# Kernel optimization log

Hardware: AMD Instinct MI355X
Metric: run time of the kernel (lower is better)

The kernel has to match this reference:

```python
import jax, jax.numpy as jnp
import numpy as np

K = 20          # hardcoded in get_graph_feature
EPS = 1e-5      # BatchNorm2d default eps


def bn(x, g, b):
    # training-mode batch norm over all axes except channel (last axis), biased var
    ax = tuple(range(x.ndim - 1))
    m = x.mean(axis=ax, keepdims=True)
    v = x.var(axis=ax, keepdims=True)
    return (x - m) * jax.lax.rsqrt(v + EPS) * g + b


def knn_idx(x):
    # x: (B, C, N) -> (B, N, K) indices of K nearest neighbors (incl. self)
    xt = jnp.swapaxes(x, 1, 2)                      # (B, N, C)
    inner = -2.0 * jnp.einsum('bnc,bmc->bnm', xt, xt)
    xx = jnp.sum(x * x, axis=1)                     # (B, N)
    neg_dist = -xx[:, :, None] - inner - xx[:, None, :]   # (B, N, N)
    _, idx = jax.lax.top_k(neg_dist, K)
    return idx


def graph_feature(x):
    # x: (B, C, N) -> (B, N, K, 2C)  [neighbor feats, center feats]
    idx = knn_idx(x)
    xt = jnp.swapaxes(x, 1, 2)                      # (B, N, C)
    B = x.shape[0]
    nb = xt[jnp.arange(B)[:, None, None], idx]      # (B, N, K, C)
    ctr = jnp.broadcast_to(xt[:, :, None, :], nb.shape)
    return jnp.concatenate([nb, ctr], axis=-1)


def setup_inputs() -> dict:
    key = jax.random.key(0)
    ks = jax.random.split(key, 12)
    B, C, N = 8, 3, 4096
    EMB = 512

    def w(k, cin, cout):
        return jax.random.normal(k, (cin, cout), dtype=jnp.float32) * np.float32(1.0 / np.sqrt(cin))

    return {
        'x': jax.random.normal(ks[0], (B, C, N), dtype=jnp.float32),
        'W1': w(ks[1], 2 * C, 64),
        'W2': w(ks[2], 64, 64),
        'W3': w(ks[3], 64, 128),
        'W4': w(ks[4], 128, 256),
        'W5': w(ks[5], 512, EMB),
        'g1': jnp.ones((64,), jnp.float32),  'b1': jnp.zeros((64,), jnp.float32),
        'g2': jnp.ones((64,), jnp.float32),  'b2': jnp.zeros((64,), jnp.float32),
        'g3': jnp.ones((128,), jnp.float32), 'b3': jnp.zeros((128,), jnp.float32),
        'g4': jnp.ones((256,), jnp.float32), 'b4': jnp.zeros((256,), jnp.float32),
        'g5': jnp.ones((EMB,), jnp.float32), 'b5': jnp.zeros((EMB,), jnp.float32),
    }


def reference(x, W1, W2, W3, W4, W5, g1, b1, g2, b2, g3, b3, g4, b4, g5, b5):
    f = graph_feature(x)                              # (B, N, K, 6)
    h = jax.nn.relu(bn(f @ W1, g1, b1))               # (B, N, K, 64)
    x1 = h.max(axis=2)                                # (B, N, 64)
    h = jax.nn.relu(bn(h @ W2, g2, b2))
    x2 = h.max(axis=2)
    h = jax.nn.relu(bn(h @ W3, g3, b3))
    x3 = h.max(axis=2)
    h = jax.nn.relu(bn(h @ W4, g4, b4))
    x4 = h.max(axis=2)                                # (B, N, 256)
    cat = jnp.concatenate([x1, x2, x3, x4], axis=-1)  # (B, N, 512)
    out = jax.nn.relu(bn(cat @ W5, g5, b5))           # (B, N, 512); last_relu=True
    return jnp.swapaxes(out, 1, 2)                    # (B, 512, N)
```

## Files before the change

### kernel.cpp

```cpp
#include <hip/hip_runtime.h>
#include <hip/hip_bf16.h>
#include <cfloat>

using bf16 = __hip_bfloat16;

typedef short short8 __attribute__((ext_vector_type(8)));
typedef float floatx16 __attribute__((ext_vector_type(16)));
union Frag { short8 v; uint2 u2[2]; };
union FragQ { short8 v; uint4 q; uint2 u2[2]; };
union U4b { uint4 q; unsigned short s[8]; };

constexpr int Bb = 8, Nn = 4096, Kk = 20;
constexpr int BN = Bb * Nn;
constexpr int Mrows = BN * Kk;
constexpr float EPSf = 1e-5f;

static __device__ __forceinline__ float b2f(bf16 v){ return __bfloat162float(v); }
static __device__ __forceinline__ bf16 f2b(float v){ return __float2bfloat16(v); }
static __device__ __forceinline__ unsigned short f2bu(float v){
  union { bf16 b; unsigned short u; } cv; cv.b = __float2bfloat16(v); return cv.u;
}
static __device__ __forceinline__ float bits2f(unsigned short u){
  union { unsigned int i; float f; } c; c.i = ((unsigned)u)<<16; return c.f;
}

__global__ void zero_kernel(float* __restrict__ p, int n){
  int i = blockIdx.x*256 + threadIdx.x;
  if (i < n) p[i] = 0.f;
}

__global__ void w3t_kernel(const float* __restrict__ W3f, bf16* __restrict__ W3T){
  int id = blockIdx.x*256 + threadIdx.x;
  if (id >= 128*64) return;
  int n = id >> 6, k = id & 63;
  W3T[id] = f2b(W3f[(size_t)k*128 + n]);
}

__global__ void w4t_kernel(const float* __restrict__ W4f, bf16* __restrict__ W4T){
  int id = blockIdx.x*256 + threadIdx.x;
  if (id >= 128*256) return;
  int k = id >> 8, c = id & 255;
  W4T[(size_t)c*128 + k] = f2b(W4f[id]);
}

__global__ void w5t_kernel(const float* __restrict__ W5f, bf16* __restrict__ W5T){
  int id = blockIdx.x*256 + threadIdx.x;
  if (id >= 512*512) return;
  int k = id >> 9, c = id & 511;
  W5T[(size_t)c*512 + k] = f2b(W5f[id]);
}

__global__ __launch_bounds__(256) void knnA_kernel(const float* __restrict__ x,
                                                   float* __restrict__ pv, int* __restrict__ pi){
#pragma clang fp contract(off)
  __shared__ float4 p4[512];
  __shared__ unsigned short lst[256*62];
  int blk = blockIdx.x;
  int stripe = blk & 7;
  int chunk  = (blk >> 3) & 15;
  int b      = blk >> 7;
  const float* xb = x + b*3*Nn;
  int j0 = stripe*512;
  for (int u = threadIdx.x; u < 512; u += 256){
    int j = j0 + u;
    float a0 = xb[j];
    float a1 = xb[Nn + j];
    float a2 = xb[2*Nn + j];
    float s = a0*a0; s = s + a1*a1; s = s + a2*a2;
    p4[u] = make_float4(a0, a1, a2, s);
  }
  __syncthreads();
  int i = chunk*256 + threadIdx.x;
  float xi = xb[i], yi = xb[Nn+i], zi = xb[2*Nn+i];
  float ni = xi*xi; ni = ni + yi*yi; ni = ni + zi*zi;
  float mni = -ni;
  float xi2 = xi + xi, yi2 = yi + yi, zi2 = zi + zi;
  float bv[13];
  #pragma unroll
  for (int s=0;s<13;++s) bv[s] = FLT_MAX;
  for (int g=0; g<32; ++g){
    float gm = -FLT_MAX;
    #pragma unroll
    for (int e=0;e<16;++e){
      float4 p = p4[g*16+e];
      float base = mni - p.w;
      float nd = fmaf(xi2, p.x, fmaf(yi2, p.y, fmaf(zi2, p.z, base)));
      gm = fmaxf(gm, nd);
    }
    #pragma unroll
    for (int s=12; s>=1; --s)
      bv[s] = fminf(bv[s], fmaxf(bv[s-1], gm));
    bv[0] = fminf(bv[0], gm);
  }
  float thr = bv[12];
  thr = thr - (fabsf(thr)*1e-5f + 1e-6f);
  unsigned short* ml = &lst[threadIdx.x*62];
  int cnt = 0;
  for (int u=0; u<512; ++u){
    float4 p = p4[u];
    float base = mni - p.w;
    float nd = fmaf(xi2, p.x, fmaf(yi2, p.y, fmaf(zi2, p.z, base)));
    if (nd >= thr && cnt < 60){ ml[cnt] = (unsigned short)u; ++cnt; }
  }
  float av[Kk]; int ai[Kk];
  #pragma unroll
  for (int s=0;s<Kk;++s){ av[s] = -FLT_MAX; ai[s] = 0; }
  if (cnt >= 60){
    for (int u=0; u<512; ++u){
      float4 p = p4[u];
      float dot = xi*p.x; dot = dot + yi*p.y; dot = dot + zi*p.z;
      float inner = -2.0f*dot;
      float nd = mni - inner; nd = nd - p.w;
      if (nd > av[Kk-1]){
        #pragma unroll
        for (int s=Kk-1; s>=1; --s){
          bool cs = nd > av[s];
          bool cp = nd > av[s-1];
          av[s] = cs ? (cp ? av[s-1] : nd) : av[s];
          ai[s] = cs ? (cp ? ai[s-1] : (j0+u)) : ai[s];
        }
        if (nd > av[0]){ av[0] = nd; ai[0] = j0+u; }
      }
    }
  } else {
    for (int t=0; t<cnt; ++t){
      int lj = ml[t];
      float4 p = p4[lj];
      float dot = xi*p.x; dot = dot + yi*p.y; dot = dot + zi*p.z;
      float inner = -2.0f*dot;
      float nd = mni - inner; nd = nd - p.w;
      if (nd > av[Kk-1]){
        #pragma unroll
        for (int s=Kk-1; s>=1; --s){
          bool cs = nd > av[s];
          bool cp = nd > av[s-1];
          av[s] = cs ? (cp ? av[s-1] : nd) : av[s];
          ai[s] = cs ? (cp ? ai[s-1] : (j0+lj)) : ai[s];
        }
        if (nd > av[0]){ av[0] = nd; ai[0] = j0+lj; }
      }
    }
  }
  long long base = ((long long)(b*Nn + i)*8 + stripe)*Kk;
  #pragma unroll
  for (int s=0;s<Kk;++s){ pv[base+s] = av[s]; pi[base+s] = ai[s]; }
}

__global__ __launch_bounds__(256) void knnB_kernel(const float* __restrict__ pv,
                                                   const int* __restrict__ pi,
                                                   const float* __restrict__ x,
                                                   int* __restrict__ idx,
                                                   float* __restrict__ part){
  int p = blockIdx.x*256 + threadIdx.x;
  long long base = (long long)p*8*Kk;
  float av[Kk]; int ai[Kk];
  #pragma unroll
  for (int s=0;s<Kk;++s){ av[s]=pv[base+s]; ai[s]=pi[base+s]; }
  for (int t=Kk; t<8*Kk; ++t){
    float nd = pv[base+t]; int j = pi[base+t];
    if (nd > av[Kk-1]){
      #pragma unroll
      for (int s=Kk-1;s>=1;--s){
        bool cs = nd > av[s];
        bool cp = nd > av[s-1];
        av[s] = cs ? (cp?av[s-1]:nd) : av[s];
        ai[s] = cs ? (cp?ai[s-1]:j) : ai[s];
      }
      if (nd > av[0]){ av[0]=nd; ai[0]=j; }
    }
  }
  #pragma unroll
  for (int s=0;s<Kk;++s) idx[(long long)p*Kk+s] = ai[s];
  int b = p >> 12, n = p & 4095;
  const float* xb = x + b*3*Nn;
  float cx = xb[n], cy = xb[Nn+n], cz = xb[2*Nn+n];
  float snx=0.f, sny=0.f, snz=0.f;
  float a00=0.f,a01=0.f,a02=0.f,a11=0.f,a12=0.f,a22=0.f;
  #pragma unroll
  for (int s=0;s<Kk;++s){
    int j = ai[s];
    float nx = xb[j], ny = xb[Nn+j], nz = xb[2*Nn+j];
    snx += nx; sny += ny; snz += nz;
    a00 = fmaf(nx,nx,a00); a01 = fmaf(nx,ny,a01); a02 = fmaf(nx,nz,a02);
    a11 = fmaf(ny,ny,a11); a12 = fmaf(ny,nz,a12); a22 = fmaf(nz,nz,a22);
  }
  float acc[36];
  acc[0]=a00;  acc[1]=a01;  acc[2]=a02;
  acc[6]=a01;  acc[7]=a11;  acc[8]=a12;
  acc[12]=a02; acc[13]=a12; acc[14]=a22;
  acc[3]=snx*cx;  acc[4]=snx*cy;  acc[5]=snx*cz;
  acc[9]=sny*cx;  acc[10]=sny*cy; acc[11]=sny*cz;
  acc[15]=snz*cx; acc[16]=snz*cy; acc[17]=snz*cz;
  acc[18]=cx*snx; acc[19]=cx*sny; acc[20]=cx*snz;
  acc[24]=cy*snx; acc[25]=cy*sny; acc[26]=cy*snz;
  acc[30]=cz*snx; acc[31]=cz*sny; acc[32]=cz*snz;
  float k20 = (float)Kk;
  acc[21]=k20*cx*cx; acc[22]=k20*cx*cy; acc[23]=k20*cx*cz;
  acc[27]=k20*cy*cx; acc[28]=k20*cy*cy; acc[29]=k20*cy*cz;
  acc[33]=k20*cz*cx; acc[34]=k20*cz*cy; acc[35]=k20*cz*cz;
  float s6[6] = { snx, sny, snz, k20*cx, k20*cy, k20*cz };
  __shared__ float red[256];
  #pragma unroll
  for (int v=0; v<42; ++v){
    red[threadIdx.x] = (v<36)? acc[v] : s6[v-36];
    __syncthreads();
    for (int s=128; s>0; s>>=1){
      if (threadIdx.x < s) red[threadIdx.x] += red[threadIdx.x+s];
      __syncthreads();
    }
    if (threadIdx.x==0) part[blockIdx.x*48 + v] = red[0];
    __syncthreads();
  }
}

__global__ void reducef_kernel(const float* __restrict__ part, float* __restrict__ Gf,
                               float* __restrict__ sumf){
  int t = threadIdx.x;
  if (t < 42){
    float s = 0.f;
    for (int i=0;i<128;++i) s += part[i*48 + t];
    if (t<36) Gf[t]=s; else sumf[t-36]=s;
  }
}

__global__ __launch_bounds__(256) void gram3_kernel(const bf16* __restrict__ H, int M,
                                                    float* __restrict__ G,
                                                    float* __restrict__ sumh){
  __shared__ short HTa[64*68];
  __shared__ float csum[64];
  int tid = threadIdx.x, lane = tid & 63, w = tid >> 6;
  if (tid < 64) csum[tid] = 0.f;
  int nchunks = gridDim.x;
  int rpc = M / nchunks;
  int r0 = blockIdx.x*rpc;
  int mt = w >> 1, nt = w & 1;
  floatx16 acc;
  #pragma unroll
  for (int q=0;q<16;++q) acc[q]=0.f;
  int arow = (mt*32 + (lane&31))*68;
  int brow = (nt*32 + (lane&31))*68;
  int ko = (lane>>5)*8;
  int c0s = (tid & 7)*8;
  float cs[8];
  #pragma unroll
  for (int j=0;j<8;++j) cs[j]=0.f;
  for (int rb=r0; rb<r0+rpc; rb+=64){
    #pragma unroll
    for (int s=0;s<2;++s){
      int e = tid + s*256;
      int row = e >> 3;
      U4b va; va.q = *(const uint4*)&H[(size_t)(rb+row)*64 + c0s];
      #pragma unroll
      for (int j=0;j<8;++j){
        HTa[(c0s+j)*68 + row] = (short)va.s[j];
        cs[j] += bits2f(va.s[j]);
      }
    }
    __syncthreads();
    #pragma unroll
    for (int kc=0;kc<64;kc+=16){
      Frag a, b;
      const short* ap = &HTa[arow + kc + ko];
      const short* bp = &HTa[brow + kc + ko];
      a.u2[0] = *(const uint2*)ap;  a.u2[1] = *(const uint2*)(ap+4);
      b.u2[0] = *(const uint2*)bp;  b.u2[1] = *(const uint2*)(bp+4);
      acc = __builtin_amdgcn_mfma_f32_32x32x16_bf16(a.v, b.v, acc, 0, 0, 0);
    }
    __syncthreads();
  }
  int col = lane & 31, rbase = 4*(lane>>5);
  #pragma unroll
  for (int r=0;r<16;++r){
    int row = (r&3) + 8*(r>>2) + rbase;
    atomicAdd(&G[(size_t)(mt*32 + row)*64 + nt*32 + col], acc[r]);
  }
  #pragma unroll
  for (int j=0;j<8;++j) atomicAdd(&csum[c0s+j], cs[j]);
  __syncthreads();
  if (tid < 64) atomicAdd(&sumh[tid], csum[tid]);
}

__global__ __launch_bounds__(256) void gram5_kernel(const bf16* __restrict__ H,
                                                    float* __restrict__ G,
                                                    float* __restrict__ sumh){
  __shared__ short HTa[128*68];
  __shared__ short HTb[128*68];
  __shared__ float csum[128];
  int blk = blockIdx.x;
  int pair = blk & 15;
  int chunk = blk >> 4;
  int tr = pair >> 2, tc = pair & 3;
  bool diag = (tr == tc);
  int tid = threadIdx.x, lane = tid & 63, w = tid >> 6;
  if (tid < 128) csum[tid] = 0.f;
  int rpc = BN / 32;
  int r0 = chunk*rpc;
  int pl = lane & 31, ko = (lane>>5)*8, rbase = 4*(lane>>5);
  int mt = w;
  int arow = (mt*32 + pl)*68;
  floatx16 acc[4];
  #pragma unroll
  for (int nt=0;nt<4;++nt)
    #pragma unroll
    for (int q=0;q<16;++q) acc[nt][q]=0.f;
  int c0s = (tid & 15)*8;
  float cs[8];
  #pragma unroll
  for (int j=0;j<8;++j) cs[j]=0.f;
  const short* Bbase = diag ? HTa : HTb;
  for (int rb=r0; rb<r0+rpc; rb+=64){
    #pragma unroll
    for (int s=0;s<4;++s){
      int e = tid + s*256;
      int row = e >> 4;
      U4b va; va.q = *(const uint4*)&H[(size_t)(rb+row)*512 + tr*128 + c0s];
      #pragma unroll
      for (int j=0;j<8;++j) HTa[(c0s+j)*68 + row] = (short)va.s[j];
      if (diag){
        #pragma unroll
        for (int j=0;j<8;++j) cs[j] += bits2f(va.s[j]);
      } else {
        U4b vb; vb.q = *(const uint4*)&H[(size_t)(rb+row)*512 + tc*128 + c0s];
        #pragma unroll
        for (int j=0;j<8;++j) HTb[(c0s+j)*68 + row] = (short)vb.s[j];
      }
    }
    __syncthreads();
    #pragma unroll
    for (int kc=0;kc<64;kc+=16){
      Frag a;
      const short* ap = &HTa[arow + kc + ko];
      a.u2[0] = *(const uint2*)ap;  a.u2[1] = *(const uint2*)(ap+4);
      #pragma unroll
      for (int nt=0;nt<4;++nt){
        Frag b;
        const short* bp = &Bbase[(nt*32 + pl)*68 + kc + ko];
        b.u2[0] = *(const uint2*)bp;  b.u2[1] = *(const uint2*)(bp+4);
        acc[nt] = __builtin_amdgcn_mfma_f32_32x32x16_bf16(a.v, b.v, acc[nt], 0, 0, 0);
      }
    }
    __syncthreads();
  }
  #pragma unroll
  for (int nt=0;nt<4;++nt){
    #pragma unroll
    for (int r=0;r<16;++r){
      int row = (r&3) + 8*(r>>2) + rbase;
      atomicAdd(&G[(size_t)(tr*128 + mt*32 + row)*512 + tc*128 + nt*32 + pl], acc[nt][r]);
    }
  }
  if (diag){
    #pragma unroll
    for (int j=0;j<8;++j) atomicAdd(&csum[c0s+j], cs[j]);
    __syncthreads();
    if (tid < 128) atomicAdd(&sumh[tr*128 + tid], csum[tid]);
  }
}

__global__ void kP_kernel(const float* __restrict__ G, const float* __restrict__ Wf,
                          float* __restrict__ P, int Cin, int Cout){
  int id = blockIdx.x*256 + threadIdx.x;
  if (id >= Cin*Cout) return;
  int i = id / Cout, j = id - i*Cout;
  float s = 0.f;
  for (int k=0;k<Cin;++k) s = fmaf(G[(size_t)i*Cin+k], Wf[(size_t)k*Cout+j], s);
  P[id] = s;
}

__global__ __launch_bounds__(256) void kP512_kernel(const float* __restrict__ G,
                                                    const float* __restrict__ Wf,
                                                    float* __restrict__ P){
  __shared__ float Gs[8][512];
  int tid = threadIdx.x;
  int r0 = (blockIdx.x >> 1) * 8;
  int j  = (blockIdx.x & 1) * 256 + tid;
  for (int u = tid; u < 8*512; u += 256)
    Gs[u >> 9][u & 511] = G[(size_t)(r0 + (u >> 9))*512 + (u & 511)];
  __syncthreads();
  float acc[8];
  #pragma unroll
  for (int i=0;i<8;++i) acc[i]=0.f;
  for (int k=0;k<512;++k){
    float wv = Wf[(size_t)k*512 + j];
    #pragma unroll
    for (int i=0;i<8;++i) acc[i] = fmaf(Gs[i][k], wv, acc[i]);
  }
  #pragma unroll
  for (int i=0;i<8;++i) P[(size_t)(r0+i)*512 + j] = acc[i];
}

__global__ __launch_bounds__(256) void kFinal_kernel(const float* __restrict__ P,
                              const float* __restrict__ sumh,
                              const float* __restrict__ Wf, const float* __restrict__ g,
                              const float* __restrict__ bb, float* __restrict__ scale,
                              float* __restrict__ shift, int Cin, int Cout, float invM){
  __shared__ float redm[256], rede[256];
  int tid = threadIdx.x;
  int j = blockIdx.x*16 + (tid & 15);
  int sub = tid >> 4;
  float mean = 0.f, e2 = 0.f;
  for (int i = sub; i < Cin; i += 16){
    float w = Wf[(size_t)i*Cout + j];
    mean = fmaf(sumh[i], w, mean);
    e2   = fmaf(w, P[(size_t)i*Cout + j], e2);
  }
  redm[tid] = mean; rede[tid] = e2;
  __syncthreads();
  for (int s = 128; s >= 16; s >>= 1){
    if (tid < s){ redm[tid] += redm[tid+s]; rede[tid] += rede[tid+s]; }
    __syncthreads();
  }
  if (tid < 16){
    float m = redm[tid]*invM, e = rede[tid]*invM;
    float var = e - m*m;
    float inv = rsqrtf(var + EPSf);
    float sc = g[j]*inv;
    scale[j] = sc;
    shift[j] = bb[j] - m*sc;
  }
}

__global__ __launch_bounds__(512) void stats2_kernel(const float* __restrict__ x,
    const int* __restrict__ idx, const float* __restrict__ W1f,
    const float* __restrict__ sc1v, const float* __restrict__ sh1v,
    float* __restrict__ G2, float* __restrict__ sum2){
  __shared__ float W1s[6][64];
  __shared__ float fsh[64][8];
  __shared__ short H1T[64*68];
  __shared__ float csum[64];
  int tid = threadIdx.x, lane = tid & 63, w = tid >> 6;
  if (tid < 384) W1s[tid>>6][tid&63] = W1f[tid];
  if (tid < 64) csum[tid] = 0.f;
  int rp = tid >> 4, cq = tid & 15, c0 = cq*4;
  float sca[4], sha[4];
  #pragma unroll
  for (int k=0;k<4;++k){ sca[k]=sc1v[c0+k]; sha[k]=sh1v[c0+k]; }
  int mt = w & 1, nt = (w>>1) & 1, kh = w >> 2;
  int arow = (mt*32 + (lane&31))*68;
  int brow = (nt*32 + (lane&31))*68;
  int ko = (lane>>5)*8;
  floatx16 acc;
  #pragma unroll
  for (int q=0;q<16;++q) acc[q]=0.f;
  float cs[4] = {0.f,0.f,0.f,0.f};
  int rpc = Mrows / gridDim.x;
  int r0 = blockIdx.x * rpc;
  __syncthreads();
  for (int rb=r0; rb<r0+rpc; rb+=64){
    {
      int r = tid>>3, e = tid&7;
      if (e < 6){
        int grow = rb + r;
        int bn = grow / Kk;
        int b = bn >> 12, n = bn & 4095;
        int j = idx[grow];
        const float* xb = x + b*3*Nn;
        fsh[r][e] = (e<3) ? xb[e*Nn + j] : xb[(e-3)*Nn + n];
      }
    }
    __syncthreads();
    {
      float y0[4]={0,0,0,0}, y1[4]={0,0,0,0};
      int ra = rp*2, rbw = rp*2+1;
      #pragma unroll
      for (int i=0;i<6;++i){
        float fa = fsh[ra][i], fb = fsh[rbw][i];
        float4 wv = *(const float4*)&W1s[i][c0];
        y0[0]=fmaf(fa,wv.x,y0[0]); y0[1]=fmaf(fa,wv.y,y0[1]);
        y0[2]=fmaf(fa,wv.z,y0[2]); y0[3]=fmaf(fa,wv.w,y0[3]);
        y1[0]=fmaf(fb,wv.x,y1[0]); y1[1]=fmaf(fb,wv.y,y1[1]);
        y1[2]=fmaf(fb,wv.z,y1[2]); y1[3]=fmaf(fb,wv.w,y1[3]);
      }
      #pragma unroll
      for (int k=0;k<4;++k){
        float va = fmaxf(fmaf(y0[k],sca[k],sha[k]),0.f);
        float vb = fmaxf(fmaf(y1[k],sca[k],sha[k]),0.f);
        cs[k] += va; cs[k] += vb;
        unsigned int pk = f2bu(va) | ((unsigned)f2bu(vb)<<16);
        *(unsigned int*)&H1T[(c0+k)*68 + ra] = pk;
      }
    }
    __syncthreads();
    {
      int kc = kh*32;
      #pragma unroll
      for (int s=0;s<2;++s){
        Frag a, b;
        const short* ap = &H1T[arow + kc + s*16 + ko];
        const short* bp = &H1T[brow + kc + s*16 + ko];
        a.u2[0] = *(const uint2*)ap;  a.u2[1] = *(const uint2*)(ap+4);
        b.u2[0] = *(const uint2*)bp;  b.u2[1] = *(const uint2*)(bp+4);
        acc = __builtin_amdgcn_mfma_f32_32x32x16_bf16(a.v, b.v, acc, 0, 0, 0);
      }
    }
    __syncthreads();
  }
  int col = lane & 31, rbase = 4*(lane>>5);
  #pragma unroll
  for (int r=0;r<16;++r){
    int row = (r&3) + 8*(r>>2) + rbase;
    atomicAdd(&G2[(size_t)(mt*32+row)*64 + nt*32+col], acc[r]);
  }
  #pragma unroll
  for (int k=0;k<4;++k) atomicAdd(&csum[c0+k], cs[k]);
  __syncthreads();
  if (tid < 64) atomicAdd(&sum2[tid], csum[tid]);
}

__global__ __launch_bounds__(64) void fl12_kernel(const float* __restrict__ x,
    const int* __restrict__ idx, const float* __restrict__ W1f,
    const float* __restrict__ sc1v, const float* __restrict__ sh1v,
    const float* __restrict__ W2f, const float* __restrict__ sc2v,
    const float* __restrict__ sh2v, bf16* __restrict__ H2, bf16* __restrict__ cat){
  __shared__ float fsh[Kk][6];
  __shared__ float h1[Kk][64];
  __shared__ float mm[4][64];
  int bn = blockIdx.x, b = bn>>12, n = bn & 4095;
  int tid = threadIdx.x;
  if (tid < Kk){
    int j = idx[(size_t)bn*Kk + tid];
    const float* xb = x + b*3*Nn;
    fsh[tid][0]=xb[j]; fsh[tid][1]=xb[Nn+j]; fsh[tid][2]=xb[2*Nn+j];
    fsh[tid][3]=xb[n]; fsh[tid][4]=xb[Nn+n]; fsh[tid][5]=xb[2*Nn+n];
  }
  __syncthreads();
  {
    float sc=sc1v[tid], sh=sh1v[tid];
    float w[6];
    #pragma unroll
    for (int i=0;i<6;++i) w[i]=W1f[i*64+tid];
    float mx = 0.f;
    #pragma unroll
    for (int r=0;r<Kk;++r){
      float y=0.f;
      #pragma unroll
      for (int i=0;i<6;++i) y = fmaf(fsh[r][i], w[i], y);
      float v = fmaxf(fmaf(y,sc,sh),0.f);
      h1[r][tid]=v;
      mx = fmaxf(mx,v);
    }
    cat[(size_t)bn*512 + tid] = f2b(mx);
  }
  __syncthreads();
  int q = tid >> 4, c0 = (tid & 15)*4;
  float acc[5][4]={};
  for (int i0=0;i0<64;i0+=4){
    float hv[5][4];
    #pragma unroll
    for (int l=0;l<5;++l){
      float4 t4 = *(const float4*)&h1[q*5+l][i0];
      hv[l][0]=t4.x; hv[l][1]=t4.y; hv[l][2]=t4.z; hv[l][3]=t4.w;
    }
    #pragma unroll
    for (int ii=0;ii<4;++ii){
      const float* wp = W2f + (i0+ii)*64 + c0;
      float w0=wp[0],w1=wp[1],w2=wp[2],w3=wp[3];
      #pragma unroll
      for (int l=0;l<5;++l){
        float hvv=hv[l][ii];
        acc[l][0]=fmaf(hvv,w0,acc[l][0]);
        acc[l][1]=fmaf(hvv,w1,acc[l][1]);
        acc[l][2]=fmaf(hvv,w2,acc[l][2]);
        acc[l][3]=fmaf(hvv,w3,acc[l][3]);
      }
    }
  }
  float sc[4],sh[4];
  #pragma unroll
  for (int cb=0;cb<4;++cb){ sc[cb]=sc2v[c0+cb]; sh[cb]=sh2v[c0+cb]; }
  float mx[4]={0,0,0,0};
  #pragma unroll
  for (int l=0;l<5;++l){
    unsigned short us[4];
    #pragma unroll
    for (int cb=0;cb<4;++cb){
      float v=fmaxf(fmaf(acc[l][cb],sc[cb],sh[cb]),0.f);
      mx[cb]=fmaxf(mx[cb],v);
      us[cb]=f2bu(v);
    }
    uint2 v2; v2.x = us[0]|((unsigned)us[1]<<16); v2.y=us[2]|((unsigned)us[3]<<16);
    *(uint2*)(H2 + ((size_t)bn*Kk + q*5+l)*64 + c0) = v2;
  }
  #pragma unroll
  for (int cb=0;cb<4;++cb) mm[q][c0+cb]=mx[cb];
  __syncthreads();
  {
    float M0 = fmaxf(fmaxf(mm[0][tid],mm[1][tid]),fmaxf(mm[2][tid],mm[3][tid]));
    cat[(size_t)bn*512 + 64 + tid] = f2b(M0);
  }
}

__global__ __launch_bounds__(512) void stats4_kernel(const bf16* __restrict__ H2,
    const bf16* __restrict__ W3T, const float* __restrict__ sc3v, const float* __restrict__ sh3v,
    float* __restrict__ G4, float* __restrict__ sum4){
  __shared__ short h2s[64*68];
  __shared__ short H3T[128*68];
  __shared__ float csum[128];
  int tid = threadIdx.x, lane = tid & 63, w = tid >> 6;
  if (tid < 128) csum[tid] = 0.f;
  int trow = tid >> 3, tc0 = (tid & 7)*8;
  int pl  = lane & 31;
  int ko  = (lane >> 5)*8;
  int pmt = w >> 2, pnt = w & 3;
  int parow = (pmt*32 + pl)*68;
  int pcol  = pnt*32 + pl;
  float psc = sc3v[pcol], psh = sh3v[pcol];
  int prbase = 4*(lane>>5);
  FragQ bfr[4];
  #pragma unroll
  for (int kq=0;kq<4;++kq)
    bfr[kq].q = *(const uint4*)&W3T[(size_t)pcol*64 + kq*16 + ko];
  int gmt = w>>1, gnt0 = (w&1)*2, gnt1 = gnt0+1;
  int garow  = (gmt*32 + pl)*68;
  int gbrow0 = (gnt0*32 + pl)*68;
  int gbrow1 = (gnt1*32 + pl)*68;
  floatx16 acc0, acc1;
  #pragma unroll
  for (int q=0;q<16;++q){ acc0[q]=0.f; acc1[q]=0.f; }
  float cs = 0.f;
  int rpc = Mrows / gridDim.x;
  int r0 = blockIdx.x * rpc;
  uint4 hreg = *(const uint4*)&H2[(size_t)(r0+trow)*64 + tc0];
  for (int rb=r0; rb<r0+rpc; rb+=64){
    {
      short* dst = &h2s[trow*68 + tc0];
      *(uint2*)dst       = make_uint2(hreg.x, hreg.y);
      *(uint2*)(dst + 4) = make_uint2(hreg.z, hreg.w);
    }
    if (rb + 64 < r0 + rpc)
      hreg = *(const uint4*)&H2[(size_t)(rb+64+trow)*64 + tc0];
    __syncthreads();
    {
      floatx16 pacc;
      #pragma unroll
      for (int q=0;q<16;++q) pacc[q]=0.f;
      #pragma unroll
      for (int kq=0;kq<4;++kq){
        Frag a;
        const short* ap = &h2s[parow + kq*16 + ko];
        a.u2[0] = *(const uint2*)ap;  a.u2[1] = *(const uint2*)(ap+4);
        pacc = __builtin_amdgcn_mfma_f32_32x32x16_bf16(a.v, bfr[kq].v, pacc, 0, 0, 0);
      }
      #pragma unroll
      for (int g=0; g<4; ++g){
        unsigned short p[4];
        #pragma unroll
        for (int r=0;r<4;++r){
          float v = fmaxf(fmaf(pacc[g*4+r], psc, psh), 0.f);
          cs += v;
          p[r] = f2bu(v);
        }
        uint2 pk; pk.x = p[0] | ((unsigned)p[1]<<16); pk.y = p[2] | ((unsigned)p[3]<<16);
        *(uint2*)&H3T[pcol*68 + pmt*32 + 8*g + prbase] = pk;
      }
    }
    __syncthreads();
    #pragma unroll
    for (int kc=0;kc<64;kc+=16){
      Frag a, b0, b1;
      const short* ap  = &H3T[garow  + kc + ko];
      const short* bp0 = &H3T[gbrow0 + kc + ko];
      const short* bp1 = &H3T[gbrow1 + kc + ko];
      a.u2[0]  = *(const uint2*)ap;   a.u2[1]  = *(const uint2*)(ap+4);
      b0.u2[0] = *(const uint2*)bp0;  b0.u2[1] = *(const uint2*)(bp0+4);
      b1.u2[0] = *(const uint2*)bp1;  b1.u2[1] = *(const uint2*)(bp1+4);
      acc0 = __builtin_amdgcn_mfma_f32_32x32x16_bf16(a.v, b0.v, acc0, 0, 0, 0);
      acc1 = __builtin_amdgcn_mfma_f32_32x32x16_bf16(a.v, b1.v, acc1, 0, 0, 0);
    }
  }
  int col = pl;
  #pragma unroll
  for (int r=0;r<16;++r){
    int row = (r&3) + 8*(r>>2) + prbase;
    atomicAdd(&G4[(size_t)(gmt*32+row)*128 + gnt0*32+col], acc0[r]);
    atomicAdd(&G4[(size_t)(gmt*32+row)*128 + gnt1*32+col], acc1[r]);
  }
  atomicAdd(&csum[pcol], cs);
  __syncthreads();
  if (tid < 128) atomicAdd(&sum4[tid], csum[tid]);
}

__global__ __launch_bounds__(512,4) void fl34_kernel(const bf16* __restrict__ H2,
    const bf16* __restrict__ W3T, const float* __restrict__ sc3v, const float* __restrict__ sh3v,
    const bf16* __restrict__ W4T, const float* __restrict__ sc4v, const float* __restrict__ sh4v,
    bf16* __restrict__ cat){
  __shared__ short h2s[64*68];
  __shared__ short h3s[64*132];
  __shared__ unsigned short h4s[64*256];
  __shared__ unsigned short mx3u[16*128];
  __shared__ unsigned short mx4u[16*256];
  int tid = threadIdx.x, lane = tid & 63, w = tid >> 6;
  int pl = lane & 31;
  int ko = (lane >> 5)*8;
  int rbase = 4*(lane>>5);
  {
    unsigned* p4 = (unsigned*)mx4u;
    for (int u=tid; u<2048; u+=512) p4[u]=0u;
    unsigned* p3 = (unsigned*)mx3u;
    for (int u=tid; u<1024; u+=512) p3[u]=0u;
  }
  int mt3 = w >> 2, ct3 = w & 3;
  int c3 = ct3*32 + pl;
  float sc3 = sc3v[c3], sh3 = sh3v[c3];
  int a3row = (mt3*32 + pl)*68;
  int c4 = w*32 + pl;
  float sc4 = sc4v[c4], sh4 = sh4v[c4];
  int trow = tid >> 3, tc0 = (tid & 7)*8;
  int r0 = blockIdx.x * 320;
  uint4 hreg = *(const uint4*)&H2[(size_t)(r0+trow)*64 + tc0];
  {
    short* dst = &h2s[trow*68 + tc0];
    *(uint2*)dst       = make_uint2(hreg.x, hreg.y);
    *(uint2*)(dst + 4) = make_uint2(hreg.z, hreg.w);
  }
  hreg = *(const uint4*)&H2[(size_t)(r0 + 64 + trow)*64 + tc0];
  __syncthreads();
  for (int t=0; t<5; ++t){
    {
      floatx16 pa;
      #pragma unroll
      for (int q=0;q<16;++q) pa[q]=0.f;
      #pragma unroll
      for (int kq=0;kq<4;++kq){
        Frag a; FragQ b;
        const short* ap = &h2s[a3row + kq*16 + ko];
        a.u2[0] = *(const uint2*)ap;  a.u2[1] = *(const uint2*)(ap+4);
        b.q = *(const uint4*)&W3T[(size_t)c3*64 + kq*16 + ko];
        pa = __builtin_amdgcn_mfma_f32_32x32x16_bf16(a.v, b.v, pa, 0, 0, 0);
      }
      #pragma unroll
      for (int r=0;r<16;++r){
        int m = mt3*32 + (r&3) + 8*(r>>2) + rbase;
        float v = fmaxf(fmaf(pa[r], sc3, sh3), 0.f);
        h3s[m*132 + c3] = (short)f2bu(v);
      }
    }
    __syncthreads();
    #pragma unroll
    for (int mt4=0; mt4<2; ++mt4){
      floatx16 acc;
      #pragma unroll
      for (int q=0;q<16;++q) acc[q]=0.f;
      int a4row = (mt4*32 + pl)*132;
      #pragma unroll
      for (int kq=0;kq<8;++kq){
        Frag a; FragQ b;
        const short* ap = &h3s[a4row + kq*16 + ko];
        a.u2[0] = *(const uint2*)ap;  a.u2[1] = *(const uint2*)(ap+4);
        b.q = *(const uint4*)&W4T[(size_t)c4*128 + kq*16 + ko];
        acc = __builtin_amdgcn_mfma_f32_32x32x16_bf16(a.v, b.v, acc, 0, 0, 0);
      }
      #pragma unroll
      for (int r=0;r<16;++r){
        int m = mt4*32 + (r&3) + 8*(r>>2) + rbase;
        float v = fmaxf(fmaf(acc[r], sc4, sh4), 0.f);
        h4s[m*256 + c4] = f2bu(v);
      }
    }
    __syncthreads();
    if (t < 4){
      short* dst = &h2s[trow*68 + tc0];
      *(uint2*)dst       = make_uint2(hreg.x, hreg.y);
      *(uint2*)(dst + 4) = make_uint2(hreg.z, hreg.w);
      if (t < 3) hreg = *(const uint4*)&H2[(size_t)(r0 + (t+2)*64 + trow)*64 + tc0];
    }
    {
      int lr0 = t*64;
      if (tid < 256){
        int c = tid;
        int p = lr0/20;
        int nb = (p+1)*20 - lr0;
        unsigned ml = 0;
        for (int r=0;r<64;++r){
          unsigned v = h4s[r*256 + c];
          ml = v > ml ? v : ml;
          if (--nb == 0){
            unsigned short* mp = &mx4u[p*256 + c];
            unsigned cur = *mp;
            if (ml > cur) *mp = (unsigned short)ml;
            ml = 0; ++p; nb = 20;
          }
        }
        if (nb != 20){
          unsigned short* mp = &mx4u[p*256 + c];
          unsigned cur = *mp;
          if (ml > cur) *mp = (unsigned short)ml;
        }
      } else if (tid < 384){
        int c = tid - 256;
        int p = lr0/20;
        int nb = (p+1)*20 - lr0;
        unsigned ml = 0;
        for (int r=0;r<64;++r){
          unsigned v = (unsigned)(unsigned short)h3s[r*132 + c];
          ml = v > ml ? v : ml;
          if (--nb == 0){
            unsigned short* mp = &mx3u[p*128 + c];
            unsigned cur = *mp;
            if (ml > cur) *mp = (unsigned short)ml;
            ml = 0; ++p; nb = 20;
          }
        }
        if (nb != 20){
          unsigned short* mp = &mx3u[p*128 + c];
          unsigned cur = *mp;
          if (ml > cur) *mp = (unsigned short)ml;
        }
      }
    }
    __syncthreads();
  }
  int bn0 = blockIdx.x*16;
  {
    int p = tid >> 5, c0 = (tid & 31)*8;
    uint4 v = *(const uint4*)&mx4u[p*256 + c0];
    *(uint4*)&cat[(size_t)(bn0+p)*512 + 256 + c0] = v;
  }
  if (tid < 256){
    int p = tid >> 4, c0 = (tid & 15)*8;
    uint4 v = *(const uint4*)&mx3u[p*128 + c0];
    *(uint4*)&cat[(size_t)(bn0+p)*512 + 128 + c0] = v;
  }
}

__global__ __launch_bounds__(512) void l5_kernel(const bf16* __restrict__ cat,
                                                const bf16* __restrict__ W5T,
                                                const float* __restrict__ scale,
                                                const float* __restrict__ shift,
                                                float* __restrict__ out){
  __shared__ float obu[64*129];
  short* cs2 = (short*)obu;
  float* ob = obu;
  int tid = threadIdx.x, lane = tid & 63, w = tid >> 6;
  int pl = lane & 31;
  int ko = (lane >> 5)*8;
  int rbase = 4*(lane>>5);
  int mt = w & 1, ntb = w >> 1;
  int arow = (mt*32 + pl)*68;
  int trow = tid >> 3, tc0 = (tid & 7)*8;
  int r0 = blockIdx.x*64;
  floatx16 acc[4];
  #pragma unroll
  for (int s=0;s<4;++s)
    #pragma unroll
    for (int q=0;q<16;++q) acc[s][q]=0.f;
  const bf16* arow_g = cat + (size_t)(r0+trow)*512 + tc0;
  uint4 hreg = *(const uint4*)arow_g;
  {
    short* dst = &cs2[trow*68 + tc0];
    *(uint2*)dst       = make_uint2(hreg.x, hreg.y);
    *(uint2*)(dst + 4) = make_uint2(hreg.z, hreg.w);
  }
  hreg = *(const uint4*)(arow_g + 64);
  __syncthreads();
  for (int kc8=0; kc8<8; ++kc8){
    int cur = kc8 & 1;
    if (kc8 < 7){
      short* dst = &cs2[(cur^1)*64*68 + trow*68 + tc0];
      *(uint2*)dst       = make_uint2(hreg.x, hreg.y);
      *(uint2*)(dst + 4) = make_uint2(hreg.z, hreg.w);
      if (kc8 < 6) hreg = *(const uint4*)(arow_g + (kc8+2)*64);
    }
    const short* csb = cs2 + cur*64*68;
    #pragma unroll
    for (int kq=0;kq<4;++kq){
      Frag a;
      const short* ap = &csb[arow + kq*16 + ko];
      a.u2[0] = *(const uint2*)ap;  a.u2[1] = *(const uint2*)(ap+4);
      #pragma unroll
      for (int s=0;s<4;++s){
        FragQ b;
        int col = (ntb + 4*s)*32 + pl;
        b.q = *(const uint4*)&W5T[(size_t)col*512 + kc8*64 + kq*16 + ko];
        acc[s] = __builtin_amdgcn_mfma_f32_32x32x16_bf16(a.v, b.v, acc[s], 0, 0, 0);
      }
    }
    __syncthreads();
  }
  int b = r0 >> 12, n0 = r0 & 4095;
  int colL = ntb*32 + pl;
  int colc = tid >> 2, sub = tid & 3;
  for (int s=0;s<4;++s){
    float sc = scale[128*s + colL], sh = shift[128*s + colL];
    #pragma unroll
    for (int q=0;q<16;++q){
      int m = mt*32 + (q&3) + 8*(q>>2) + rbase;
      ob[m*129 + colL] = fmaxf(fmaf(acc[s][q], sc, sh), 0.f);
    }
    __syncthreads();
    float* op = out + ((size_t)b*512 + 128*s + colc)*4096 + n0 + sub*16;
    #pragma unroll
    for (int j=0;j<4;++j){
      int rr = sub*16 + j*4;
      float4 v = make_float4(ob[(rr+0)*129 + colc], ob[(rr+1)*129 + colc],
                             ob[(rr+2)*129 + colc], ob[(rr+3)*129 + colc]);
      *(float4*)(op + j*4) = v;
    }
    __syncthreads();
  }
}

extern "C" void kernel_launch(void* const* d_in, const int* in_sizes, int n_in,
                              void* d_out, int out_size, void* d_ws, size_t ws_size,
                              hipStream_t stream){
  const float* x   = (const float*)d_in[0];
  const float* W1f = (const float*)d_in[1];
  const float* W2f = (const float*)d_in[2];
  const float* W3f = (const float*)d_in[3];
  const float* W4f = (const float*)d_in[4];
  const float* W5f = (const float*)d_in[5];
  const float* g1=(const float*)d_in[6],  *b1=(const float*)d_in[7];
  const float* g2=(const float*)d_in[8],  *b2=(const float*)d_in[9];
  const float* g3=(const float*)d_in[10], *b3=(const float*)d_in[11];
  const float* g4=(const float*)d_in[12], *b4=(const float*)d_in[13];
  const float* g5=(const float*)d_in[14], *b5=(const float*)d_in[15];
  float* out = (float*)d_out;

  char* w = (char*)d_ws;
  size_t off = 0;
  auto alloc = [&](size_t bytes)->void*{
    void* p = w + off;
    off = (off + bytes + 255) & ~(size_t)255;
    return p;
  };

  int*  idxb = (int*) alloc((size_t)BN*Kk*4);
  bf16* H2   = (bf16*)alloc((size_t)Mrows*64*2);
  bf16* catb = (bf16*)alloc((size_t)BN*512*2);
  bf16* W3T  = (bf16*)alloc((size_t)128*64*2);
  bf16* W4T  = (bf16*)alloc((size_t)256*128*2);
  bf16* W5T  = (bf16*)alloc((size_t)512*512*2);
  float* pv  = (float*)H2;
  int*   pib = (int*)((char*)H2 + (size_t)BN*8*Kk*4);

  size_t statsStart = off;
  float* partf=(float*)alloc(256*48*4);
  float* Gf=(float*)alloc(36*4);
  float* sumf=(float*)alloc(8*4);
  float* G2=(float*)alloc(4096*4);   float* sum2=(float*)alloc(64*4);
  float* G3=(float*)alloc(4096*4);   float* sum3=(float*)alloc(64*4);
  float* G4=(float*)alloc(16384*4);  float* sum4=(float*)alloc(128*4);
  float* G5=(float*)alloc(262144*4); float* sum5=(float*)alloc(512*4);
  float* P1=(float*)alloc(384*4);
  float* P2=(float*)alloc(4096*4);
  float* P3=(float*)alloc(8192*4);
  float* P4=(float*)alloc(32768*4);
  float* P5=(float*)alloc(262144*4);
  float* sc1=(float*)alloc(64*4);   float* sh1=(float*)alloc(64*4);
  float* sc2=(float*)alloc(64*4);   float* sh2=(float*)alloc(64*4);
  float* sc3=(float*)alloc(128*4);  float* sh3=(float*)alloc(128*4);
  float* sc4=(float*)alloc(256*4);  float* sh4=(float*)alloc(256*4);
  float* sc5=(float*)alloc(512*4);  float* sh5=(float*)alloc(512*4);
  size_t statsEnd = off;

  int statsFloats = (int)((statsEnd - statsStart)/4);
  zero_kernel<<<(statsFloats+255)/256,256,0,stream>>>((float*)(w+statsStart), statsFloats);
  w3t_kernel<<<32,256,0,stream>>>(W3f, W3T);
  w4t_kernel<<<128,256,0,stream>>>(W4f, W4T);
  w5t_kernel<<<1024,256,0,stream>>>(W5f, W5T);

  knnA_kernel<<<1024,256,0,stream>>>(x, pv, pib);
  knnB_kernel<<<BN/256,256,0,stream>>>(pv, pib, x, idxb, partf);

  const float invM  = 1.0f/(float)Mrows;
  const float invM5 = 1.0f/(float)BN;

  reducef_kernel<<<1,64,0,stream>>>(partf, Gf, sumf);
  kP_kernel<<<2,256,0,stream>>>(Gf, W1f, P1, 6, 64);
  kFinal_kernel<<<4,256,0,stream>>>(P1, sumf, W1f, g1, b1, sc1, sh1, 6, 64, invM);

  stats2_kernel<<<512,512,0,stream>>>(x, idxb, W1f, sc1, sh1, G2, sum2);
  kP_kernel<<<16,256,0,stream>>>(G2, W2f, P2, 64, 64);
  kFinal_kernel<<<4,256,0,stream>>>(P2, sum2, W2f, g2, b2, sc2, sh2, 64, 64, invM);

  fl12_kernel<<<BN,64,0,stream>>>(x, idxb, W1f, sc1, sh1, W2f, sc2, sh2, H2, catb);

  gram3_kernel<<<512,256,0,stream>>>(H2, Mrows, G3, sum3);
  kP_kernel<<<32,256,0,stream>>>(G3, W3f, P3, 64, 128);
  kFinal_kernel<<<8,256,0,stream>>>(P3, sum3, W3f, g3, b3, sc3, sh3, 64, 128, invM);

  stats4_kernel<<<512,512,0,stream>>>(H2, W3T, sc3, sh3, G4, sum4);
  kP_kernel<<<128,256,0,stream>>>(G4, W4f, P4, 128, 256);
  kFinal_kernel<<<16,256,0,stream>>>(P4, sum4, W4f, g4, b4, sc4, sh4, 128, 256, invM);

  fl34_kernel<<<Mrows/320,512,0,stream>>>(H2, W3T, sc3, sh3, W4T, sc4, sh4, catb);

  gram5_kernel<<<512,256,0,stream>>>(catb, G5, sum5);
  kP512_kernel<<<128,256,0,stream>>>(G5, W5f, P5);
  kFinal_kernel<<<32,256,0,stream>>>(P5, sum5, W5f, g5, b5, sc5, sh5, 512, 512, invM5);
  l5_kernel<<<BN/64,512,0,stream>>>(catb, W5T, sc5, sh5, out);
}
```

Before: 976.2 us.

## Rewrite fl12 kernel to use MFMA for layer 2 over 320-row tiles

The layer-1/2 fused kernel moves from one 64-thread block per point, with scalar FP32 FMAs for the 64x64 matmul, to 512-thread blocks that each handle 16 points (320 rows) in five 64-row tiles. Layer 1 is computed into bf16 shared memory, layer 2 runs on bf16 MFMA 32x32x16 using a pre-transposed W2, and per-point maxima are kept in shared memory as bf16 bit patterns. The aim is to cut the FP32 ALU cost and the overhead of tiny blocks. In exchange, the h1 activations now go into the layer-2 matmul rounded to bf16. During the MFMA phase only four of the eight waves do matmul work, one wave does the layer-1 max, and the rest wait at the barrier.

```diff
diff --git a/kernel.cpp b/kernel.cpp
--- a/kernel.cpp
+++ b/kernel.cpp
@@ -27,6 +27,13 @@
 __global__ void zero_kernel(float* __restrict__ p, int n){
   int i = blockIdx.x*256 + threadIdx.x;
   if (i < n) p[i] = 0.f;
+}
+
+__global__ void w2t_kernel(const float* __restrict__ W2f, bf16* __restrict__ W2T){
+  int id = blockIdx.x*256 + threadIdx.x;
+  if (id >= 64*64) return;
+  int n = id >> 6, k = id & 63;
+  W2T[id] = f2b(W2f[(size_t)k*64 + n]);
 }
 
 __global__ void w3t_kernel(const float* __restrict__ W3f, bf16* __restrict__ W3T){
@@ -507,86 +514,162 @@
   if (tid < 64) atomicAdd(&sum2[tid], csum[tid]);
 }
 
-__global__ __launch_bounds__(64) void fl12_kernel(const float* __restrict__ x,
+__global__ __launch_bounds__(512) void fl12_kernel(const float* __restrict__ x,
     const int* __restrict__ idx, const float* __restrict__ W1f,
     const float* __restrict__ sc1v, const float* __restrict__ sh1v,
-    const float* __restrict__ W2f, const float* __restrict__ sc2v,
+    const bf16* __restrict__ W2T, const float* __restrict__ sc2v,
     const float* __restrict__ sh2v, bf16* __restrict__ H2, bf16* __restrict__ cat){
-  __shared__ float fsh[Kk][6];
-  __shared__ float h1[Kk][64];
-  __shared__ float mm[4][64];
-  int bn = blockIdx.x, b = bn>>12, n = bn & 4095;
-  int tid = threadIdx.x;
-  if (tid < Kk){
-    int j = idx[(size_t)bn*Kk + tid];
-    const float* xb = x + b*3*Nn;
-    fsh[tid][0]=xb[j]; fsh[tid][1]=xb[Nn+j]; fsh[tid][2]=xb[2*Nn+j];
-    fsh[tid][3]=xb[n]; fsh[tid][4]=xb[Nn+n]; fsh[tid][5]=xb[2*Nn+n];
-  }
+  __shared__ float W1s[6][64];
+  __shared__ float fsh[64][8];
+  __shared__ short h1s[64*68];
+  __shared__ short h2sT[64*68];
+  __shared__ unsigned short mx1u[16*64];
+  __shared__ unsigned short mx2u[16*64];
+  int tid = threadIdx.x, lane = tid & 63, w = tid >> 6;
+  int pl = lane & 31;
+  int ko = (lane >> 5)*8;
+  int rbase = 4*(lane>>5);
+  if (tid < 384) W1s[tid>>6][tid&63] = W1f[tid];
+  {
+    unsigned* p1 = (unsigned*)mx1u;
+    unsigned* p2 = (unsigned*)mx2u;
+    for (int u=tid; u<512; u+=512){ p1[u]=0u; p2[u]=0u; }
+  }
+  int rp = tid >> 4, cq = tid & 15, c0 = cq*4;
+  float sca1[4], sha1[4];
+  #pragma unroll
+  for (int k=0;k<4;++k){ sca1[k]=sc1v[c0+k]; sha1[k]=sh1v[c0+k]; }
+  int mt = (w>>1)&1, nt = w&1;
+  int pcol = nt*32 + pl;
+  float sca2 = sc2v[pcol], sha2 = sh2v[pcol];
+  FragQ bfr[4];
+  #pragma unroll
+  for (int kq=0;kq<4;++kq)
+    bfr[kq].q = *(const uint4*)&W2T[(size_t)pcol*64 + kq*16 + ko];
+  int a2row = (mt*32 + pl)*68;
+  int r0 = blockIdx.x * 320;
+  int bn0 = blockIdx.x * 16;
   __syncthreads();
-  {
-    float sc=sc1v[tid], sh=sh1v[tid];
-    float w[6];
-    #pragma unroll
-    for (int i=0;i<6;++i) w[i]=W1f[i*64+tid];
-    float mx = 0.f;
-    #pragma unroll
-    for (int r=0;r<Kk;++r){
-      float y=0.f;
-      #pragma unroll
-      for (int i=0;i<6;++i) y = fmaf(fsh[r][i], w[i], y);
-      float v = fmaxf(fmaf(y,sc,sh),0.f);
-      h1[r][tid]=v;
-      mx = fmaxf(mx,v);
-    }
-    cat[(size_t)bn*512 + tid] = f2b(mx);
-  }
-  __syncthreads();
-  int q = tid >> 4, c0 = (tid & 15)*4;
-  float acc[5][4]={};
-  for (int i0=0;i0<64;i0+=4){
-    float hv[5][4];
-    #pragma unroll
-    for (int l=0;l<5;++l){
-      float4 t4 = *(const float4*)&h1[q*5+l][i0];
-      hv[l][0]=t4.x; hv[l][1]=t4.y; hv[l][2]=t4.z; hv[l][3]=t4.w;
-    }
-    #pragma unroll
-    for (int ii=0;ii<4;++ii){
-      const float* wp = W2f + (i0+ii)*64 + c0;
-      float w0=wp[0],w1=wp[1],w2=wp[2],w3=wp[3];
-      #pragma unroll
-      for (int l=0;l<5;++l){
-        float hvv=hv[l][ii];
-        acc[l][0]=fmaf(hvv,w0,acc[l][0]);
-        acc[l][1]=fmaf(hvv,w1,acc[l][1]);
-        acc[l][2]=fmaf(hvv,w2,acc[l][2]);
-        acc[l][3]=fmaf(hvv,w3,acc[l][3]);
-      }
-    }
-  }
-  float sc[4],sh[4];
-  #pragma unroll
-  for (int cb=0;cb<4;++cb){ sc[cb]=sc2v[c0+cb]; sh[cb]=sh2v[c0+cb]; }
-  float mx[4]={0,0,0,0};
-  #pragma unroll
-  for (int l=0;l<5;++l){
-    unsigned short us[4];
-    #pragma unroll
-    for (int cb=0;cb<4;++cb){
-      float v=fmaxf(fmaf(acc[l][cb],sc[cb],sh[cb]),0.f);
-      mx[cb]=fmaxf(mx[cb],v);
-      us[cb]=f2bu(v);
-    }
-    uint2 v2; v2.x = us[0]|((unsigned)us[1]<<16); v2.y=us[2]|((unsigned)us[3]<<16);
-    *(uint2*)(H2 + ((size_t)bn*Kk + q*5+l)*64 + c0) = v2;
-  }
-  #pragma unroll
-  for (int cb=0;cb<4;++cb) mm[q][c0+cb]=mx[cb];
-  __syncthreads();
-  {
-    float M0 = fmaxf(fmaxf(mm[0][tid],mm[1][tid]),fmaxf(mm[2][tid],mm[3][tid]));
-    cat[(size_t)bn*512 + 64 + tid] = f2b(M0);
+  for (int t=0; t<5; ++t){
+    int g0 = r0 + t*64;
+    {
+      int r = tid>>3, e = tid&7;
+      if (e < 6){
+        int grow = g0 + r;
+        int bn = grow / Kk;
+        int b = bn >> 12, n = bn & 4095;
+        int j = idx[grow];
+        const float* xb = x + b*3*Nn;
+        fsh[r][e] = (e<3) ? xb[e*Nn + j] : xb[(e-3)*Nn + n];
+      }
+    }
+    __syncthreads();
+    {
+      float y0[4]={0,0,0,0}, y1[4]={0,0,0,0};
+      int ra = rp*2, rb = rp*2+1;
+      #pragma unroll
+      for (int i=0;i<6;++i){
+        float fa = fsh[ra][i], fb = fsh[rb][i];
+        float4 wv = *(const float4*)&W1s[i][c0];
+        y0[0]=fmaf(fa,wv.x,y0[0]); y0[1]=fmaf(fa,wv.y,y0[1]);
+        y0[2]=fmaf(fa,wv.z,y0[2]); y0[3]=fmaf(fa,wv.w,y0[3]);
+        y1[0]=fmaf(fb,wv.x,y1[0]); y1[1]=fmaf(fb,wv.y,y1[1]);
+        y1[2]=fmaf(fb,wv.z,y1[2]); y1[3]=fmaf(fb,wv.w,y1[3]);
+      }
+      unsigned short ua[4], ub[4];
+      #pragma unroll
+      for (int k=0;k<4;++k){
+        ua[k] = f2bu(fmaxf(fmaf(y0[k],sca1[k],sha1[k]),0.f));
+        ub[k] = f2bu(fmaxf(fmaf(y1[k],sca1[k],sha1[k]),0.f));
+      }
+      uint2 va; va.x = ua[0]|((unsigned)ua[1]<<16); va.y = ua[2]|((unsigned)ua[3]<<16);
+      uint2 vb; vb.x = ub[0]|((unsigned)ub[1]<<16); vb.y = ub[2]|((unsigned)ub[3]<<16);
+      *(uint2*)&h1s[ra*68 + c0] = va;
+      *(uint2*)&h1s[rb*68 + c0] = vb;
+    }
+    __syncthreads();
+    if (w < 4){
+      floatx16 pacc;
+      #pragma unroll
+      for (int q=0;q<16;++q) pacc[q]=0.f;
+      #pragma unroll
+      for (int kq=0;kq<4;++kq){
+        Frag a;
+        const short* ap = &h1s[a2row + kq*16 + ko];
+        a.u2[0] = *(const uint2*)ap;  a.u2[1] = *(const uint2*)(ap+4);
+        pacc = __builtin_amdgcn_mfma_f32_32x32x16_bf16(a.v, bfr[kq].v, pacc, 0, 0, 0);
+      }
+      #pragma unroll
+      for (int g=0; g<4; ++g){
+        unsigned short p[4];
+        #pragma unroll
+        for (int r=0;r<4;++r)
+          p[r] = f2bu(fmaxf(fmaf(pacc[g*4+r], sca2, sha2), 0.f));
+        uint2 pk; pk.x = p[0] | ((unsigned)p[1]<<16); pk.y = p[2] | ((unsigned)p[3]<<16);
+        *(uint2*)&h2sT[pcol*68 + mt*32 + 8*g + rbase] = pk;
+      }
+    } else if (w == 4){
+      int c = tid - 256;
+      int lr0 = t*64;
+      int p = lr0/20;
+      int nb = (p+1)*20 - lr0;
+      unsigned ml = 0;
+      for (int r=0;r<64;++r){
+        unsigned v = (unsigned)(unsigned short)h1s[r*68 + c];
+        ml = v > ml ? v : ml;
+        if (--nb == 0){
+          unsigned short* mp = &mx1u[p*64 + c];
+          unsigned cur = *mp;
+          if (ml > cur) *mp = (unsigned short)ml;
+          ml = 0; ++p; nb = 20;
+        }
+      }
+      if (nb != 20){
+        unsigned short* mp = &mx1u[p*64 + c];
+        unsigned cur = *mp;
+        if (ml > cur) *mp = (unsigned short)ml;
+      }
+    }
+    __syncthreads();
+    {
+      int row = tid >> 3, cc0 = (tid & 7)*8;
+      unsigned short us[8];
+      #pragma unroll
+      for (int j=0;j<8;++j) us[j] = (unsigned short)h2sT[(cc0+j)*68 + row];
+      uint4 v; v.x = us[0]|((unsigned)us[1]<<16); v.y = us[2]|((unsigned)us[3]<<16);
+      v.z = us[4]|((unsigned)us[5]<<16); v.w = us[6]|((unsigned)us[7]<<16);
+      *(uint4*)&H2[(size_t)(g0+row)*64 + cc0] = v;
+    }
+    if (tid < 64){
+      int c = tid;
+      int lr0 = t*64;
+      int p = lr0/20;
+      int nb = (p+1)*20 - lr0;
+      unsigned ml = 0;
+      for (int r=0;r<64;++r){
+        unsigned v = (unsigned)(unsigned short)h2sT[c*68 + r];
+        ml = v > ml ? v : ml;
+        if (--nb == 0){
+          unsigned short* mp = &mx2u[p*64 + c];
+          unsigned cur = *mp;
+          if (ml > cur) *mp = (unsigned short)ml;
+          ml = 0; ++p; nb = 20;
+        }
+      }
+      if (nb != 20){
+        unsigned short* mp = &mx2u[p*64 + c];
+        unsigned cur = *mp;
+        if (ml > cur) *mp = (unsigned short)ml;
+      }
+    }
+    __syncthreads();
+  }
+  if (tid < 256){
+    int p = tid >> 4, cc0 = (tid & 15)*4;
+    uint2 v1 = *(const uint2*)&mx1u[p*64 + cc0];
+    *(uint2*)&cat[(size_t)(bn0+p)*512 + cc0] = v1;
+    uint2 v2 = *(const uint2*)&mx2u[p*64 + cc0];
+    *(uint2*)&cat[(size_t)(bn0+p)*512 + 64 + cc0] = v2;
   }
 }
 
@@ -927,6 +1010,7 @@
   int*  idxb = (int*) alloc((size_t)BN*Kk*4);
   bf16* H2   = (bf16*)alloc((size_t)Mrows*64*2);
   bf16* catb = (bf16*)alloc((size_t)BN*512*2);
+  bf16* W2T  = (bf16*)alloc((size_t)64*64*2);
   bf16* W3T  = (bf16*)alloc((size_t)128*64*2);
   bf16* W4T  = (bf16*)alloc((size_t)256*128*2);
   bf16* W5T  = (bf16*)alloc((size_t)512*512*2);
@@ -955,6 +1039,7 @@
 
   int statsFloats = (int)((statsEnd - statsStart)/4);
   zero_kernel<<<(statsFloats+255)/256,256,0,stream>>>((float*)(w+statsStart), statsFloats);
+  w2t_kernel<<<16,256,0,stream>>>(W2f, W2T);
   w3t_kernel<<<32,256,0,stream>>>(W3f, W3T);
   w4t_kernel<<<128,256,0,stream>>>(W4f, W4T);
   w5t_kernel<<<1024,256,0,stream>>>(W5f, W5T);
@@ -973,7 +1058,7 @@
   kP_kernel<<<16,256,0,stream>>>(G2, W2f, P2, 64, 64);
   kFinal_kernel<<<4,256,0,stream>>>(P2, sum2, W2f, g2, b2, sc2, sh2, 64, 64, invM);
 
-  fl12_kernel<<<BN,64,0,stream>>>(x, idxb, W1f, sc1, sh1, W2f, sc2, sh2, H2, catb);
+  fl12_kernel<<<Mrows/320,512,0,stream>>>(x, idxb, W1f, sc1, sh1, W2T, sc2, sh2, H2, catb);
 
   gram3_kernel<<<512,256,0,stream>>>(H2, Mrows, G3, sum3);
   kP_kernel<<<32,256,0,stream>>>(G3, W3f, P3, 64, 128);
```

New measurement: 1.013 ms. +3.7%, slower.
